# Kernel optimization log

Measured on AMD Instinct MI355X. Metric: run time of the kernel, lower is better.

Reference implementation:

```python
import jax, jax.numpy as jnp
import numpy as np

N_NODES = 200000
N_EDGES = 3200000
NUM_FEATURES = 165
HIDDEN = 128
NUM_CLASSES = 2
K = 3  # Chebyshev order for both convs


def setup_inputs() -> dict:
    key = jax.random.key(0)
    k1, k2, k3, k4, k5 = jax.random.split(key, 5)
    x = jax.random.normal(k1, (N_NODES, NUM_FEATURES), dtype=jnp.float32)
    edge_index = jax.random.randint(k2, (2, N_EDGES), 0, N_NODES, dtype=jnp.int64)
    # ChebConv params: K stacked [in, out] weight matrices + bias (Glorot-ish scale)
    W1 = jax.random.normal(k3, (K, NUM_FEATURES, HIDDEN), dtype=jnp.float32) / np.sqrt(NUM_FEATURES)
    b1 = jnp.zeros((HIDDEN,), dtype=jnp.float32)
    W2 = jax.random.normal(k4, (K, HIDDEN, NUM_CLASSES), dtype=jnp.float32) / np.sqrt(HIDDEN)
    b2 = jnp.zeros((NUM_CLASSES,), dtype=jnp.float32)
    return {"x": x, "edge_index": edge_index, "W1": W1, "b1": b1, "W2": W2, "b2": b2}


def _cheb_conv(x, edge_index, W, b):
    """PyG ChebConv with normalization='sym', lambda_max=2.0.
    Scaled Laplacian L_hat = 2L/lambda_max - I = -D^{-1/2} A D^{-1/2}.
    """
    n = x.shape[0]
    row, col = edge_index[0], edge_index[1]
    deg = jax.ops.segment_sum(jnp.ones(row.shape, x.dtype), row, num_segments=n)
    dis = jnp.where(deg > 0, jax.lax.rsqrt(jnp.maximum(deg, 1.0)), 0.0)
    norm = -dis[row] * dis[col]  # [E] edge weights of L_hat (diag entries are 0)

    def prop(h):  # h: [N, F] -> L_hat @ h via gather-multiply-scatter
        return jax.ops.segment_sum(norm[:, None] * h[col], row, num_segments=n)

    Tx0 = x
    out = Tx0 @ W[0]
    if W.shape[0] > 1:
        Tx1 = prop(Tx0)
        out = out + Tx1 @ W[1]
        for k in range(2, W.shape[0]):
            Tx2 = 2.0 * prop(Tx1) - Tx0
            out = out + Tx2 @ W[k]
            Tx0, Tx1 = Tx1, Tx2
    return out + b


def reference(x, edge_index, W1, b1, W2, b2):
    h = jax.nn.relu(_cheb_conv(x, edge_index, W1, b1))
    # F.dropout(training=self.training): identity in eval mode (deterministic reference)
    out = _cheb_conv(h, edge_index, W2, b2)
    return out
```

## Files before the change

### kernel.cpp

```cpp
#include <hip/hip_runtime.h>
#include <hip/hip_bf16.h>
#include <stdint.h>

#define NF 165
#define NH 128
#define KP 192
#define NCOLS 384
#define BSH 8
#define BROWS 256
#define BCAP 6144
#define NSUB 8
#define BSUBCAP 768
#define CPAD 16
#define TILE 8192
#define NBKMAX 1024

typedef __attribute__((ext_vector_type(8))) short bf16x8;
typedef __attribute__((ext_vector_type(4))) float f32x4;


__device__ __forceinline__ unsigned short f2bf(float f) {
    unsigned int u = __builtin_bit_cast(unsigned int, f);
    u = (u + 0x7FFFu + ((u >> 16) & 1u)) >> 16;
    return (unsigned short)u;
}
__device__ __forceinline__ float bf2f_lo(unsigned int v) {
    return __builtin_bit_cast(float, v << 16);
}
__device__ __forceinline__ float bf2f_hi(unsigned int v) {
    return __builtin_bit_cast(float, v & 0xFFFF0000u);
}

#define ACC8(acc, v)                                                   \
    {                                                                  \
        unsigned _vv[4] = {(v).x, (v).y, (v).z, (v).w};                \
        _Pragma("unroll") for (int _j = 0; _j < 4; ++_j) {             \
            acc[2 * _j] += bf2f_lo(_vv[_j]);                           \
            acc[2 * _j + 1] += bf2f_hi(_vv[_j]);                       \
        }                                                              \
    }


__global__ __launch_bounds__(256) void k_bucket(
        const int* __restrict__ erow, const int* __restrict__ ecol,
        int* __restrict__ bcur, unsigned int* __restrict__ bkt, int E) {
    __shared__ int hist[NBKMAX];
    __shared__ int basex[NBKMAX];
    __shared__ int gbase[NBKMAX];
    __shared__ int cur[NBKMAX];
    __shared__ int scanbuf[256];
    __shared__ unsigned stage[TILE];
    __shared__ unsigned short bof[TILE];

    int t = threadIdx.x;
    int x = blockIdx.x & (NSUB - 1);
    int e0 = blockIdx.x * TILE;
    int cnt = E - e0;
    if (cnt > TILE) cnt = TILE;
    if (cnt <= 0) return;

    for (int i = t; i < NBKMAX; i += 256) { hist[i] = 0; cur[i] = 0; }
    __syncthreads();

    for (int i = t; i < cnt; i += 256) {
        int r = __builtin_nontemporal_load(erow + e0 + i);
        atomicAdd(&hist[r >> BSH], 1);
    }
    __syncthreads();

    int b0 = 4 * t;
    int h0 = hist[b0], h1 = hist[b0 + 1], h2 = hist[b0 + 2], h3 = hist[b0 + 3];
    int tsum = h0 + h1 + h2 + h3;
    scanbuf[t] = tsum;
    __syncthreads();
#pragma unroll
    for (int ofs = 1; ofs < 256; ofs <<= 1) {
        int v = (t >= ofs) ? scanbuf[t - ofs] : 0;
        __syncthreads();
        scanbuf[t] += v;
        __syncthreads();
    }
    int excl = scanbuf[t] - tsum;
    basex[b0] = excl;
    basex[b0 + 1] = excl + h0;
    basex[b0 + 2] = excl + h0 + h1;
    basex[b0 + 3] = excl + h0 + h1 + h2;
    int hb[4] = {h0, h1, h2, h3};
#pragma unroll
    for (int j = 0; j < 4; ++j) {
        int b = b0 + j;
        if (hb[j] > 0)
            gbase[b] = atomicAdd(&bcur[(b * NSUB + x) * CPAD], hb[j]);
    }
    __syncthreads();

    for (int i = t; i < cnt; i += 256) {
        int r = __builtin_nontemporal_load(erow + e0 + i);
        int c = __builtin_nontemporal_load(ecol + e0 + i);
        int b = r >> BSH;
        int rk = atomicAdd(&cur[b], 1);
        int pos = basex[b] + rk;
        stage[pos] = ((unsigned)(r & (BROWS - 1)) << 18) | (unsigned)c;
        bof[pos] = (unsigned short)b;
    }
    __syncthreads();

    for (int i = t; i < cnt; i += 256) {
        int b = bof[i];
        int slot = gbase[b] + (i - basex[b]);
        if (slot < BSUBCAP)
            bkt[(size_t)(b * NSUB + x) * BSUBCAP + slot] = stage[i];
    }
}

__global__ __launch_bounds__(256) void k_hist(
        const int* __restrict__ bcur, const unsigned int* __restrict__ bkt,
        int* __restrict__ cnt, float* __restrict__ dis, int N) {
    __shared__ int h[BROWS];
    int b = blockIdx.x;
    int t = threadIdx.x;
    h[t] = 0;
    __syncthreads();
#pragma unroll
    for (int x = 0; x < NSUB; ++x) {
        int sub = b * NSUB + x;
        int nb = bcur[sub * CPAD];
        if (nb > BSUBCAP) nb = BSUBCAP;
        const unsigned int* src = bkt + (size_t)sub * BSUBCAP;
        for (int i = t; i < nb; i += 256)
            atomicAdd(&h[__builtin_nontemporal_load(src + i) >> 18], 1);
    }
    __syncthreads();
    int base = b << BSH;
    if (base + t < N) {
        int d = h[t];
        cnt[base + t] = d;
        dis[base + t] = (d > 0) ? rsqrtf((float)d) : 0.0f;
    }
}

__global__ __launch_bounds__(256) void k_scan1(
        const int* __restrict__ cnt, int* __restrict__ off,
        int* __restrict__ bsum, int N) {
    __shared__ int sh[256];
    int t = threadIdx.x;
    int base = blockIdx.x * 1024 + t * 4;
    int v0 = (base + 0 < N) ? cnt[base + 0] : 0;
    int v1 = (base + 1 < N) ? cnt[base + 1] : 0;
    int v2 = (base + 2 < N) ? cnt[base + 2] : 0;
    int v3 = (base + 3 < N) ? cnt[base + 3] : 0;
    int tsum = v0 + v1 + v2 + v3;
    sh[t] = tsum;
    __syncthreads();
#pragma unroll
    for (int ofs = 1; ofs < 256; ofs <<= 1) {
        int x = (t >= ofs) ? sh[t - ofs] : 0;
        __syncthreads();
        sh[t] += x;
        __syncthreads();
    }
    int excl = sh[t] - tsum;
    if (t == 255) bsum[blockIdx.x] = sh[t];
    if (base + 0 < N) off[base + 0] = excl;
    excl += v0;
    if (base + 1 < N) off[base + 1] = excl;
    excl += v1;
    if (base + 2 < N) off[base + 2] = excl;
    excl += v2;
    if (base + 3 < N) off[base + 3] = excl;
}

__global__ __launch_bounds__(256) void k_scan2(int* __restrict__ bsum, int NB) {
    __shared__ int sh[256];
    int t = threadIdx.x;
    int v = (t < NB) ? bsum[t] : 0;
    sh[t] = v;
    __syncthreads();
#pragma unroll
    for (int ofs = 1; ofs < 256; ofs <<= 1) {
        int x = (t >= ofs) ? sh[t - ofs] : 0;
        __syncthreads();
        sh[t] += x;
        __syncthreads();
    }
    if (t < NB) bsum[t] = sh[t] - v;
}

__global__ __launch_bounds__(256) void k_scan3(
        int* __restrict__ off, const int* __restrict__ bsum, int N, int E) {
    int i = blockIdx.x * 256 + threadIdx.x;
    if (i >= N) return;
    off[i] = off[i] + bsum[i >> 10];
    if (i == 0) off[N] = E;
}

__global__ __launch_bounds__(256) void k_emit(
        const int* __restrict__ bcur, const unsigned int* __restrict__ bkt,
        const int* __restrict__ off, int* __restrict__ scol, int N) {
    __shared__ unsigned colbuf[BCAP];
    __shared__ int rowoff[BROWS + 1];
    __shared__ int cursor[BROWS];

    int b = blockIdx.x;
    int base = b << BSH;
    int nrows = N - base;
    if (nrows > BROWS) nrows = BROWS;
    int t = threadIdx.x;

    for (int i = t; i <= nrows; i += 256) rowoff[i] = off[base + i];
    if (t < BROWS) cursor[t] = 0;
    __syncthreads();

    int regionStart = rowoff[0];
    int total = rowoff[nrows] - regionStart;

#pragma unroll
    for (int x = 0; x < NSUB; ++x) {
        int sub = b * NSUB + x;
        int nb = bcur[sub * CPAD];
        if (nb > BSUBCAP) nb = BSUBCAP;
        const unsigned int* src = bkt + (size_t)sub * BSUBCAP;
        for (int i = t; i < nb; i += 256) {
            unsigned v = __builtin_nontemporal_load(src + i);
            int rl = v >> 18;
            unsigned c = v & 0x3FFFFu;
            int pos = (rowoff[rl] - regionStart) + atomicAdd(&cursor[rl], 1);
            if (pos < BCAP) colbuf[pos] = c;
        }
    }
    __syncthreads();

    for (int i = t; i < total; i += 256) scol[regionStart + i] = (int)colbuf[i];
}


__global__ __launch_bounds__(256) void k_xb(
        const float* __restrict__ x, unsigned short* __restrict__ xb, int N) {
    int gid = blockIdx.x * 256 + threadIdx.x;
    if (gid >= N * (KP / 8)) return;
    int row = gid / (KP / 8);
    int k0 = (gid % (KP / 8)) * 8;
    unsigned short v[8];
#pragma unroll
    for (int i = 0; i < 8; ++i) {
        int k = k0 + i;
        v[i] = (k < NF) ? f2bf(x[(size_t)row * NF + k]) : (unsigned short)0;
    }
    uint4 pk;
    pk.x = (unsigned)v[0] | ((unsigned)v[1] << 16);
    pk.y = (unsigned)v[2] | ((unsigned)v[3] << 16);
    pk.z = (unsigned)v[4] | ((unsigned)v[5] << 16);
    pk.w = (unsigned)v[6] | ((unsigned)v[7] << 16);
    *(uint4*)(xb + (size_t)row * KP + k0) = pk;
}

__global__ __launch_bounds__(256) void k_wbt(
        const float* __restrict__ W1, unsigned short* __restrict__ wbt) {
    int gid = blockIdx.x * 256 + threadIdx.x;
    if (gid >= NCOLS * (KP / 8)) return;
    int col = gid / (KP / 8);
    int k0 = (gid % (KP / 8)) * 8;
    int cc = col & 127;
    unsigned short v[8];
#pragma unroll
    for (int i = 0; i < 8; ++i) {
        int k = k0 + i;
        float f = 0.0f;
        if (k < NF) {
            if (col < 128)      f = W1[k * 128 + cc] - W1[42240 + k * 128 + cc];
            else if (col < 256) f = W1[21120 + k * 128 + cc];
            else                f = W1[42240 + k * 128 + cc];
        }
        v[i] = f2bf(f);
    }
    uint4 pk;
    pk.x = (unsigned)v[0] | ((unsigned)v[1] << 16);
    pk.y = (unsigned)v[2] | ((unsigned)v[3] << 16);
    pk.z = (unsigned)v[4] | ((unsigned)v[5] << 16);
    pk.w = (unsigned)v[6] | ((unsigned)v[7] << 16);
    *(uint4*)(wbt + (size_t)col * KP + k0) = pk;
}

__global__ __launch_bounds__(256) void k_wc2t(const float* __restrict__ W2,
                                              float* __restrict__ Wc2t) {
    int gid = blockIdx.x * 256 + threadIdx.x;
    if (gid >= 8 * 128) return;
    int t = gid >> 7;
    int k = gid & 127;
    float v = 0.0f;
    if (t < 2)      v = W2[k * 2 + t] - W2[512 + k * 2 + t];
    else if (t < 4) v = W2[256 + k * 2 + (t - 2)];
    else if (t < 6) v = W2[512 + k * 2 + (t - 4)];
    Wc2t[gid] = v;
}

__global__ __launch_bounds__(256) void k_gemm1_mfma(
        const unsigned short* __restrict__ xb, const unsigned short* __restrict__ wbt,
        const float* __restrict__ dis,
        unsigned int* __restrict__ ub, unsigned int* __restrict__ sA,
        unsigned int* __restrict__ wb, int N, int P) {
    int xcd = blockIdx.x & 7;
    int wrk = blockIdx.x >> 3;
    int p = xcd + 8 * (wrk / 3);
    int g = wrk - 3 * (wrk / 3);
    if (p >= P) return;

    __shared__ unsigned short As[128][40];
    __shared__ unsigned short Bs[128][40];

    int tid = threadIdx.x;
    int w = tid >> 6;
    int lane = tid & 63;
    int l15 = lane & 15;
    int l16 = lane >> 4;
    int brow = p * 128;
    int gcol = g * 128;

    int sr = tid >> 1;
    int sk = (tid & 1) * 16;

    f32x4 acc[2][8] = {};

    for (int kc = 0; kc < 6; ++kc) {
        int k0 = kc * 32;
        uint4 va0 = {0, 0, 0, 0}, va1 = {0, 0, 0, 0};
        if (brow + sr < N) {
            const unsigned short* asrc = xb + (size_t)(brow + sr) * KP + k0 + sk;
            va0 = *(const uint4*)asrc;
            va1 = *(const uint4*)(asrc + 8);
        }
        const unsigned short* bsrc = wbt + (size_t)(gcol + sr) * KP + k0 + sk;
        uint4 vb0 = *(const uint4*)bsrc;
        uint4 vb1 = *(const uint4*)(bsrc + 8);
        __syncthreads();
        *(uint4*)&As[sr][sk] = va0;
        *(uint4*)&As[sr][sk + 8] = va1;
        *(uint4*)&Bs[sr][sk] = vb0;
        *(uint4*)&Bs[sr][sk + 8] = vb1;
        __syncthreads();

        bf16x8 a[2], b[8];
#pragma unroll
        for (int m = 0; m < 2; ++m)
            a[m] = *(const bf16x8*)&As[w * 32 + m * 16 + l15][l16 * 8];
#pragma unroll
        for (int n = 0; n < 8; ++n)
            b[n] = *(const bf16x8*)&Bs[n * 16 + l15][l16 * 8];
#pragma unroll
        for (int m = 0; m < 2; ++m)
#pragma unroll
            for (int n = 0; n < 8; ++n)
                acc[m][n] = __builtin_amdgcn_mfma_f32_16x16x32_bf16(
                    a[m], b[n], acc[m][n], 0, 0, 0);
    }

    unsigned int* dst = (g == 0) ? ub : (g == 1) ? sA : wb;
#pragma unroll
    for (int m = 0; m < 2; ++m) {
#pragma unroll
        for (int reg = 0; reg < 4; ++reg) {
            int row = brow + w * 32 + m * 16 + l16 * 4 + reg;
            if (row >= N) continue;
            float sc = (g == 0) ? 1.0f : dis[row];
#pragma unroll
            for (int n = 0; n < 4; ++n) {
                int c = n * 16 + l15;
                float lo = sc * acc[m][n][reg];
                float hi = sc * acc[m][n + 4][reg];
                dst[(size_t)row * 64 + c] =
                    (unsigned)f2bf(lo) | ((unsigned)f2bf(hi) << 16);
            }
        }
    }
}


__global__ __launch_bounds__(256) void k_prop_b2b(
        const int* __restrict__ off, const int* __restrict__ scol,
        const unsigned int* __restrict__ srcb, const unsigned int* __restrict__ addb,
        const float* __restrict__ dis, unsigned int* __restrict__ dstb, int N) {
    int wid = (blockIdx.x * 256 + threadIdx.x) >> 6;
    int lane = threadIdx.x & 63;
    int g = lane >> 4, q = lane & 15;
    int r = wid * 4 + g;
    if (r >= N) return;
    int e = off[r], end = off[r + 1];
    const uint4* src4 = (const uint4*)srcb;
    float a[8] = {}, b[8] = {};
    for (; e + 4 <= end; e += 4) {
        int c0 = scol[e], c1 = scol[e + 1], c2 = scol[e + 2], c3 = scol[e + 3];
        uint4 v0 = src4[(size_t)c0 * 16 + q];
        uint4 v1 = src4[(size_t)c1 * 16 + q];
        uint4 v2 = src4[(size_t)c2 * 16 + q];
        uint4 v3 = src4[(size_t)c3 * 16 + q];
        ACC8(a, v0);
        ACC8(b, v1);
        ACC8(a, v2);
        ACC8(b, v3);
    }
    for (; e < end; ++e) {
        int c0 = scol[e];
        uint4 v0 = src4[(size_t)c0 * 16 + q];
        ACC8(a, v0);
    }
    float d = dis[r];
    float m2 = -2.0f * d * d;
    uint4 ad = ((const uint4*)addb)[(size_t)r * 16 + q];
    unsigned adp[4] = {ad.x, ad.y, ad.z, ad.w};
    uint4 o;
    unsigned* op = (unsigned*)&o;
#pragma unroll
    for (int j = 0; j < 4; ++j) {
        float lo = bf2f_lo(adp[j]) + m2 * (a[2 * j] + b[2 * j]);
        float hi = bf2f_hi(adp[j]) + m2 * (a[2 * j + 1] + b[2 * j + 1]);
        op[j] = (unsigned)f2bf(lo) | ((unsigned)f2bf(hi) << 16);
    }
    ((uint4*)dstb)[(size_t)r * 16 + q] = o;
}

__global__ __launch_bounds__(256) void k_prop_b2f_gemm2(
        const int* __restrict__ off, const int* __restrict__ scol,
        const unsigned int* __restrict__ srcb, const unsigned int* __restrict__ addb,
        const float* __restrict__ dis, const float* __restrict__ b1,
        const float* __restrict__ Wc2t, const float* __restrict__ b2,
        float* __restrict__ out, float* __restrict__ s2, float* __restrict__ w2,
        int N) {
    __shared__ float Ws[8 * 128];
    int tid = threadIdx.x;
    for (int idx = tid; idx < 8 * 128; idx += 256) Ws[idx] = Wc2t[idx];
    __syncthreads();

    int wid = (blockIdx.x * 256 + tid) >> 6;
    int lane = tid & 63;
    int g = lane >> 4, q = lane & 15;
    int r = wid * 4 + g;
    if (r >= N) return;

    float blo[4], bhi[4];
#pragma unroll
    for (int j = 0; j < 4; ++j) {
        blo[j] = b1[q * 4 + j];
        bhi[j] = b1[q * 4 + j + 64];
    }

    int e = off[r], end = off[r + 1];
    const uint4* src4 = (const uint4*)srcb;
    float a[8] = {}, b[8] = {};
    for (; e + 4 <= end; e += 4) {
        int c0 = scol[e], c1 = scol[e + 1], c2 = scol[e + 2], c3 = scol[e + 3];
        uint4 v0 = src4[(size_t)c0 * 16 + q];
        uint4 v1 = src4[(size_t)c1 * 16 + q];
        uint4 v2 = src4[(size_t)c2 * 16 + q];
        uint4 v3 = src4[(size_t)c3 * 16 + q];
        ACC8(a, v0);
        ACC8(b, v1);
        ACC8(a, v2);
        ACC8(b, v3);
    }
    for (; e < end; ++e) {
        int c0 = scol[e];
        uint4 v0 = src4[(size_t)c0 * 16 + q];
        ACC8(a, v0);
    }
    float m1 = -dis[r];
    uint4 ad = ((const uint4*)addb)[(size_t)r * 16 + q];
    unsigned adp[4] = {ad.x, ad.y, ad.z, ad.w};
    float acc[6] = {};
#pragma unroll
    for (int j = 0; j < 4; ++j) {
        int c = q * 4 + j;
        float lo = fmaxf(bf2f_lo(adp[j]) + m1 * (a[2 * j] + b[2 * j]) + blo[j], 0.0f);
        float hi = fmaxf(bf2f_hi(adp[j]) + m1 * (a[2 * j + 1] + b[2 * j + 1]) + bhi[j], 0.0f);
#pragma unroll
        for (int t = 0; t < 6; ++t)
            acc[t] += lo * Ws[t * 128 + c] + hi * Ws[t * 128 + c + 64];
    }
#pragma unroll
    for (int ofs = 8; ofs; ofs >>= 1) {
#pragma unroll
        for (int t = 0; t < 6; ++t)
            acc[t] += __shfl_xor(acc[t], ofs);
    }
    if (q == 0) {
        float d = dis[r];
        out[(size_t)r * 2 + 0] = acc[0] + b2[0];
        out[(size_t)r * 2 + 1] = acc[1] + b2[1];
        s2[(size_t)r * 2 + 0] = d * acc[2];
        s2[(size_t)r * 2 + 1] = d * acc[3];
        w2[(size_t)r * 2 + 0] = d * acc[4];
        w2[(size_t)r * 2 + 1] = d * acc[5];
    }
}

__global__ __launch_bounds__(256) void k_prop2_csr(
        const int* __restrict__ off, const int* __restrict__ scol,
        const float* __restrict__ src, const float* __restrict__ add,
        const float* __restrict__ dis, float* __restrict__ dst,
        int sq, int N) {
    int r = blockIdx.x * 256 + threadIdx.x;
    if (r >= N) return;
    int e0 = off[r], e1 = off[r + 1];
    float a0 = 0.0f, a1 = 0.0f, b0 = 0.0f, b1v = 0.0f;
    int e = e0;
    for (; e + 2 <= e1; e += 2) {
        int c0 = scol[e], c1 = scol[e + 1];
        float2 v0 = *(const float2*)(src + (size_t)c0 * 2);
        float2 v1 = *(const float2*)(src + (size_t)c1 * 2);
        a0 += v0.x; a1 += v0.y;
        b0 += v1.x; b1v += v1.y;
    }
    if (e < e1) {
        int c0 = scol[e];
        float2 v0 = *(const float2*)(src + (size_t)c0 * 2);
        a0 += v0.x; a1 += v0.y;
    }
    a0 += b0; a1 += b1v;
    float d = dis[r];
    float m = sq ? (-2.0f * d * d) : (-d);
    float2 ad = *(const float2*)(add + (size_t)r * 2);
    float2 o = {ad.x + m * a0, ad.y + m * a1};
    *(float2*)(dst + (size_t)r * 2) = o;
}

extern "C" void kernel_launch(void* const* d_in, const int* in_sizes, int n_in,
                              void* d_out, int out_size, void* d_ws, size_t ws_size,
                              hipStream_t stream) {
    const float* x   = (const float*)d_in[0];
    const int* eidx  = (const int*)d_in[1];
    const float* W1  = (const float*)d_in[2];
    const float* b1  = (const float*)d_in[3];
    const float* W2  = (const float*)d_in[4];
    const float* b2  = (const float*)d_in[5];
    float* out       = (float*)d_out;

    int N = in_sizes[0] / NF;
    int E = in_sizes[1] / 2;
    const int* erow = eidx;
    const int* ecol = eidx + E;
    int NBK = (N + BROWS - 1) >> BSH;

    char* p = (char*)d_ws;
    auto alloc = [&](size_t bytes) {
        char* q = p;
        p += (bytes + 255) & ~(size_t)255;
        return q;
    };
    unsigned int* ub = (unsigned int*)alloc((size_t)N * 64 * 4);
    unsigned int* sA = (unsigned int*)alloc((size_t)N * 64 * 4);
    unsigned int* wb = (unsigned int*)alloc((size_t)N * 64 * 4);
    unsigned int* sb = (unsigned int*)alloc((size_t)N * 64 * 4);
    unsigned short* xb  = (unsigned short*)alloc((size_t)N * KP * 2);
    unsigned short* wbt = (unsigned short*)alloc((size_t)NCOLS * KP * 2);
    float* dis  = (float*)alloc((size_t)N * 4);
    int* cnt    = (int*)alloc((size_t)N * 4);
    int* off    = (int*)alloc((size_t)(N + 1) * 4);
    int* bsum   = (int*)alloc((size_t)256 * 4);
    int* bcur   = (int*)alloc((size_t)NBK * NSUB * CPAD * 4);
    unsigned int* bkt = (unsigned int*)alloc((size_t)NBK * NSUB * BSUBCAP * 4);
    int* scol   = (int*)alloc((size_t)E * 4);
    float* Wc2t = (float*)alloc((size_t)8 * 128 * 4);
    float* s2   = (float*)alloc((size_t)N * 2 * 4);
    float* w2   = (float*)alloc((size_t)N * 2 * 4);

    hipMemsetAsync(bcur, 0, (size_t)NBK * NSUB * CPAD * 4, stream);

    int gN = (N + 255) / 256;
    int NB = (N + 1023) / 1024;

    k_xb<<<(N * (KP / 8) + 255) / 256, 256, 0, stream>>>(x, xb, N);
    k_wbt<<<(NCOLS * (KP / 8) + 255) / 256, 256, 0, stream>>>(W1, wbt);
    k_wc2t<<<4, 256, 0, stream>>>(W2, Wc2t);

    int gT = (E + TILE - 1) / TILE;
    k_bucket<<<gT, 256, 0, stream>>>(erow, ecol, bcur, bkt, E);
    k_hist<<<NBK, 256, 0, stream>>>(bcur, bkt, cnt, dis, N);
    k_scan1<<<NB, 256, 0, stream>>>(cnt, off, bsum, N);
    k_scan2<<<1, 256, 0, stream>>>(bsum, NB);
    k_scan3<<<gN, 256, 0, stream>>>(off, bsum, N, E);
    k_emit<<<NBK, 256, 0, stream>>>(bcur, bkt, off, scol, N);

    int P = (N + 127) / 128;
    int wPerX = 3 * ((P + 7) / 8);
    k_gemm1_mfma<<<8 * wPerX, 256, 0, stream>>>(xb, wbt, dis, ub, sA, wb, N, P);

    int nw4 = (N + 3) / 4;
    int gP4 = (nw4 * 64 + 255) / 256;
    k_prop_b2b<<<gP4, 256, 0, stream>>>(off, scol, wb, sA, dis, sb, N);
    k_prop_b2f_gemm2<<<gP4, 256, 0, stream>>>(off, scol, sb, ub, dis, b1,
                                              Wc2t, b2, out, s2, w2, N);

    k_prop2_csr<<<gN, 256, 0, stream>>>(off, scol, w2, s2, dis, s2, 1, N);
    k_prop2_csr<<<gN, 256, 0, stream>>>(off, scol, s2, out, dis, out, 0, N);
}
```

Baseline: 547.0 us.

## Fuse CSR histogram, scan and emit into bucket-scan plus single emit kernel

Replaces the five-kernel CSR build (histogram, three-level scan, emit) with a single-block scan over per-bucket counts and one emit kernel. The emit kernel stages each bucket's entries in shared memory once, builds the per-row histogram, scans it locally, and writes offsets, degree normalization and sorted columns. This removes a second read of the bucket buffer, the cnt array round trip and three launches. In exchange it uses more shared memory per block (two 6144-entry buffers), which may lower occupancy, and adds a serial single-block scan.

```diff
diff --git a/kernel.cpp b/kernel.cpp
--- a/kernel.cpp
+++ b/kernel.cpp
@@ -113,124 +113,122 @@
     }
 }
 
-__global__ __launch_bounds__(256) void k_hist(
+__global__ __launch_bounds__(256) void k_bscan(
+        const int* __restrict__ bcur, int* __restrict__ boff,
+        int* __restrict__ off, int NBK, int N, int E) {
+    __shared__ int scanbuf[256];
+    int t = threadIdx.x;
+    int tot[4];
+    int tsum = 0;
+#pragma unroll
+    for (int j = 0; j < 4; ++j) {
+        int b = 4 * t + j;
+        int s = 0;
+        if (b < NBK) {
+#pragma unroll
+            for (int x = 0; x < NSUB; ++x) {
+                int nb = bcur[(b * NSUB + x) * CPAD];
+                if (nb > BSUBCAP) nb = BSUBCAP;
+                s += nb;
+            }
+        }
+        tot[j] = s;
+        tsum += s;
+    }
+    scanbuf[t] = tsum;
+    __syncthreads();
+#pragma unroll
+    for (int ofs = 1; ofs < 256; ofs <<= 1) {
+        int v = (t >= ofs) ? scanbuf[t - ofs] : 0;
+        __syncthreads();
+        scanbuf[t] += v;
+        __syncthreads();
+    }
+    int excl = scanbuf[t] - tsum;
+#pragma unroll
+    for (int j = 0; j < 4; ++j) {
+        int b = 4 * t + j;
+        if (b < NBK) boff[b] = excl;
+        excl += tot[j];
+    }
+    if (t == 255) off[N] = E;
+}
+
+__global__ __launch_bounds__(256) void k_emit2(
         const int* __restrict__ bcur, const unsigned int* __restrict__ bkt,
-        int* __restrict__ cnt, float* __restrict__ dis, int N) {
+        const int* __restrict__ boff, int* __restrict__ off,
+        float* __restrict__ dis, int* __restrict__ scol, int N) {
+    __shared__ unsigned stage[BCAP];
+    __shared__ unsigned colbuf[BCAP];
     __shared__ int h[BROWS];
+    __shared__ int rowex[BROWS];
+    __shared__ int scanbuf[256];
+    __shared__ int subofs[NSUB + 1];
+
     int b = blockIdx.x;
     int t = threadIdx.x;
-    h[t] = 0;
-    __syncthreads();
-#pragma unroll
-    for (int x = 0; x < NSUB; ++x) {
-        int sub = b * NSUB + x;
-        int nb = bcur[sub * CPAD];
-        if (nb > BSUBCAP) nb = BSUBCAP;
-        const unsigned int* src = bkt + (size_t)sub * BSUBCAP;
-        for (int i = t; i < nb; i += 256)
-            atomicAdd(&h[__builtin_nontemporal_load(src + i) >> 18], 1);
-    }
-    __syncthreads();
-    int base = b << BSH;
-    if (base + t < N) {
-        int d = h[t];
-        cnt[base + t] = d;
-        dis[base + t] = (d > 0) ? rsqrtf((float)d) : 0.0f;
-    }
-}
-
-__global__ __launch_bounds__(256) void k_scan1(
-        const int* __restrict__ cnt, int* __restrict__ off,
-        int* __restrict__ bsum, int N) {
-    __shared__ int sh[256];
-    int t = threadIdx.x;
-    int base = blockIdx.x * 1024 + t * 4;
-    int v0 = (base + 0 < N) ? cnt[base + 0] : 0;
-    int v1 = (base + 1 < N) ? cnt[base + 1] : 0;
-    int v2 = (base + 2 < N) ? cnt[base + 2] : 0;
-    int v3 = (base + 3 < N) ? cnt[base + 3] : 0;
-    int tsum = v0 + v1 + v2 + v3;
-    sh[t] = tsum;
-    __syncthreads();
-#pragma unroll
-    for (int ofs = 1; ofs < 256; ofs <<= 1) {
-        int x = (t >= ofs) ? sh[t - ofs] : 0;
-        __syncthreads();
-        sh[t] += x;
-        __syncthreads();
-    }
-    int excl = sh[t] - tsum;
-    if (t == 255) bsum[blockIdx.x] = sh[t];
-    if (base + 0 < N) off[base + 0] = excl;
-    excl += v0;
-    if (base + 1 < N) off[base + 1] = excl;
-    excl += v1;
-    if (base + 2 < N) off[base + 2] = excl;
-    excl += v2;
-    if (base + 3 < N) off[base + 3] = excl;
-}
-
-__global__ __launch_bounds__(256) void k_scan2(int* __restrict__ bsum, int NB) {
-    __shared__ int sh[256];
-    int t = threadIdx.x;
-    int v = (t < NB) ? bsum[t] : 0;
-    sh[t] = v;
-    __syncthreads();
-#pragma unroll
-    for (int ofs = 1; ofs < 256; ofs <<= 1) {
-        int x = (t >= ofs) ? sh[t - ofs] : 0;
-        __syncthreads();
-        sh[t] += x;
-        __syncthreads();
-    }
-    if (t < NB) bsum[t] = sh[t] - v;
-}
-
-__global__ __launch_bounds__(256) void k_scan3(
-        int* __restrict__ off, const int* __restrict__ bsum, int N, int E) {
-    int i = blockIdx.x * 256 + threadIdx.x;
-    if (i >= N) return;
-    off[i] = off[i] + bsum[i >> 10];
-    if (i == 0) off[N] = E;
-}
-
-__global__ __launch_bounds__(256) void k_emit(
-        const int* __restrict__ bcur, const unsigned int* __restrict__ bkt,
-        const int* __restrict__ off, int* __restrict__ scol, int N) {
-    __shared__ unsigned colbuf[BCAP];
-    __shared__ int rowoff[BROWS + 1];
-    __shared__ int cursor[BROWS];
-
-    int b = blockIdx.x;
     int base = b << BSH;
     int nrows = N - base;
     if (nrows > BROWS) nrows = BROWS;
-    int t = threadIdx.x;
-
-    for (int i = t; i <= nrows; i += 256) rowoff[i] = off[base + i];
-    if (t < BROWS) cursor[t] = 0;
-    __syncthreads();
-
-    int regionStart = rowoff[0];
-    int total = rowoff[nrows] - regionStart;
+
+    if (t == 0) {
+        int run = 0;
+#pragma unroll
+        for (int x = 0; x < NSUB; ++x) {
+            subofs[x] = run;
+            int nb = bcur[(b * NSUB + x) * CPAD];
+            if (nb > BSUBCAP) nb = BSUBCAP;
+            run += nb;
+        }
+        subofs[NSUB] = run;
+    }
+    h[t] = 0;
+    __syncthreads();
+    int total = subofs[NSUB];
 
 #pragma unroll
     for (int x = 0; x < NSUB; ++x) {
-        int sub = b * NSUB + x;
-        int nb = bcur[sub * CPAD];
-        if (nb > BSUBCAP) nb = BSUBCAP;
-        const unsigned int* src = bkt + (size_t)sub * BSUBCAP;
-        for (int i = t; i < nb; i += 256) {
-            unsigned v = __builtin_nontemporal_load(src + i);
-            int rl = v >> 18;
-            unsigned c = v & 0x3FFFFu;
-            int pos = (rowoff[rl] - regionStart) + atomicAdd(&cursor[rl], 1);
-            if (pos < BCAP) colbuf[pos] = c;
-        }
-    }
-    __syncthreads();
-
-    for (int i = t; i < total; i += 256) scol[regionStart + i] = (int)colbuf[i];
+        int o = subofs[x];
+        int n = subofs[x + 1] - o;
+        const unsigned int* src = bkt + (size_t)(b * NSUB + x) * BSUBCAP;
+        for (int i = t; i < n; i += 256)
+            stage[o + i] = __builtin_nontemporal_load(src + i);
+    }
+    __syncthreads();
+
+    for (int i = t; i < total; i += 256)
+        atomicAdd(&h[stage[i] >> 18], 1);
+    __syncthreads();
+
+    int hv = h[t];
+    scanbuf[t] = hv;
+    __syncthreads();
+#pragma unroll
+    for (int ofs = 1; ofs < 256; ofs <<= 1) {
+        int v = (t >= ofs) ? scanbuf[t - ofs] : 0;
+        __syncthreads();
+        scanbuf[t] += v;
+        __syncthreads();
+    }
+    int excl = scanbuf[t] - hv;
+    rowex[t] = excl;
+    if (t < nrows) {
+        off[base + t] = boff[b] + excl;
+        dis[base + t] = (hv > 0) ? rsqrtf((float)hv) : 0.0f;
+    }
+    h[t] = 0;
+    __syncthreads();
+
+    for (int i = t; i < total; i += 256) {
+        unsigned v = stage[i];
+        int rl = v >> 18;
+        int pos = rowex[rl] + atomicAdd(&h[rl], 1);
+        colbuf[pos] = v & 0x3FFFFu;
+    }
+    __syncthreads();
+
+    int gs = boff[b];
+    for (int i = t; i < total; i += 256) scol[gs + i] = (int)colbuf[i];
 }
 
 
@@ -552,9 +550,8 @@
     unsigned short* xb  = (unsigned short*)alloc((size_t)N * KP * 2);
     unsigned short* wbt = (unsigned short*)alloc((size_t)NCOLS * KP * 2);
     float* dis  = (float*)alloc((size_t)N * 4);
-    int* cnt    = (int*)alloc((size_t)N * 4);
     int* off    = (int*)alloc((size_t)(N + 1) * 4);
-    int* bsum   = (int*)alloc((size_t)256 * 4);
+    int* boff   = (int*)alloc((size_t)(NBK + 1) * 4);
     int* bcur   = (int*)alloc((size_t)NBK * NSUB * CPAD * 4);
     unsigned int* bkt = (unsigned int*)alloc((size_t)NBK * NSUB * BSUBCAP * 4);
     int* scol   = (int*)alloc((size_t)E * 4);
@@ -565,7 +562,6 @@
     hipMemsetAsync(bcur, 0, (size_t)NBK * NSUB * CPAD * 4, stream);
 
     int gN = (N + 255) / 256;
-    int NB = (N + 1023) / 1024;
 
     k_xb<<<(N * (KP / 8) + 255) / 256, 256, 0, stream>>>(x, xb, N);
     k_wbt<<<(NCOLS * (KP / 8) + 255) / 256, 256, 0, stream>>>(W1, wbt);
@@ -573,11 +569,8 @@
 
     int gT = (E + TILE - 1) / TILE;
     k_bucket<<<gT, 256, 0, stream>>>(erow, ecol, bcur, bkt, E);
-    k_hist<<<NBK, 256, 0, stream>>>(bcur, bkt, cnt, dis, N);
-    k_scan1<<<NB, 256, 0, stream>>>(cnt, off, bsum, N);
-    k_scan2<<<1, 256, 0, stream>>>(bsum, NB);
-    k_scan3<<<gN, 256, 0, stream>>>(off, bsum, N, E);
-    k_emit<<<NBK, 256, 0, stream>>>(bcur, bkt, off, scol, N);
+    k_bscan<<<1, 256, 0, stream>>>(bcur, boff, off, NBK, N, E);
+    k_emit2<<<NBK, 256, 0, stream>>>(bcur, bkt, boff, off, dis, scol, N);
 
     int P = (N + 127) / 128;
     int wPerX = 3 * ((P + 7) / 8);
```

Result: no change. 544.3 us (-0.5%).
